# Kernel optimization log

Hardware: AMD Instinct MI355X
Metric: run time of the kernel (lower is better)

The kernel has to match this reference:

```python
import jax, jax.numpy as jnp
import numpy as np

N_HEADS = 8
HEAD_DIM = 32
KSIZE = 3
IN_CH = 128
OUT_CH = 256


def setup_inputs() -> dict:
    key = jax.random.key(0)
    k1, k2, k3, k4 = jax.random.split(key, 4)
    x = jax.random.normal(k1, (8, IN_CH, 64, 64), dtype=jnp.float32)
    w_key = jax.random.normal(k2, (N_HEADS * HEAD_DIM, IN_CH), dtype=jnp.float32) * 0.05
    b_key = jax.random.normal(k3, (N_HEADS * HEAD_DIM,), dtype=jnp.float32) * 0.05
    # memory init in torch: uniform in [-1, 1)
    memory = jax.random.uniform(k4, (N_HEADS, HEAD_DIM * KSIZE * KSIZE, OUT_CH // N_HEADS),
                                dtype=jnp.float32) * 2.0 - 1.0
    return {"x": x, "w_key": w_key, "b_key": b_key, "memory": memory}


def _unfold(z, k):
    # z: [b, C, Hp, Wp] padded; returns [b, C*k*k, H*W] with torch.unfold layout
    b, C, Hp, Wp = z.shape
    H, W = Hp - k + 1, Wp - k + 1
    patches = [z[:, :, i:i + H, j:j + W] for i in range(k) for j in range(k)]
    # stack -> [b, C, k*k, H, W]; channel-major like torch unfold (C outer, kh*k+kw inner)
    p = jnp.stack(patches, axis=2)
    return p.reshape(b, C * k * k, H * W)


def reference(x, w_key, b_key, memory):
    b, c_in, H, W = x.shape
    k = KSIZE
    m = N_HEADS
    # 1x1 conv (to_mem_key)
    key_map = jnp.einsum('oi,bihw->bohw', w_key, x) + b_key[None, :, None, None]
    # ZeroPad2d((k//2, k%2, k//2, k%2)) = (left, right, top, bottom)
    pl, pr = k // 2, k % 2
    padded = jnp.pad(key_map, ((0, 0), (0, 0), (pl, pr), (pl, pr)))
    unf = _unfold(padded, k)                      # [b, C*k*k, L], C = m*head_dim
    ckk = unf.shape[1]
    L = unf.shape[2]
    c = ckk // m
    # rearrange 'b (c m) l -> b m c l' (m is the FAST factor, per einops pattern)
    attn = unf.reshape(b, c, m, L).transpose(0, 2, 1, 3)   # [b, m, c, L]
    attn = jax.nn.softmax(attn, axis=2)
    out = jnp.einsum('nki,bnkl->bnil', memory, attn)       # [b, m, head_out, L]
    # rearrange 'b m c (h w) -> b (m c) h w'
    return out.reshape(b, m * out.shape[2], H, W)
```

## Files before the change

kernel.cpp:

```cpp
#include <hip/hip_runtime.h>
#include <hip/hip_bf16.h>

#define B_   8
#define CIN  128
#define CKEY 256
#define NH   8
#define HOUT 32
#define CPH  288
#define HW   4096

#define ESTR   264
#define EROW   (66 * ESTR)
#define E2_BYTES   (4 * EROW * 2)
#define XROW_DW    (64 * 68)
#define SMEM_BYTES E2_BYTES

typedef __attribute__((ext_vector_type(8))) short bf16x8;
typedef __attribute__((ext_vector_type(4))) float f32x4;

static __device__ __forceinline__ unsigned bfpack2(float a, float b) {
  __hip_bfloat162 h = __float22bfloat162_rn(float2{a, b});
  unsigned r;
  __builtin_memcpy(&r, &h, 4);
  return r;
}
static __device__ __forceinline__ unsigned short f2bf(float f) {
  unsigned u = __builtin_bit_cast(unsigned, f);
  u += 0x7FFFu + ((u >> 16) & 1u);
  return (unsigned short)(u >> 16);
}

__global__ __launch_bounds__(256) void prep_kernel(
    const float* __restrict__ mem, unsigned short* __restrict__ mfragP)
{
  const int idx  = blockIdx.x * 256 + threadIdx.x;
  const int lane = idx & 63, fi = idx >> 6;
  const int ib = fi & 1, pm = fi >> 1;
  const int p = pm % 9, m = pm / 9;
  const int li = lane & 15, q = lane >> 4;
  const int i = ib * 16 + li;
  unsigned short* dst = mfragP + (size_t)idx * 8;
#pragma unroll
  for (int j = 0; j < 8; ++j) {
    const int s = q * 8 + j;
    const int c = ((m - p + 8) & 7) + 8 * s;
    const int t = (9 * c + p) >> 3;
    dst[j] = f2bf(mem[((size_t)m * CPH + t) * HOUT + i]);
  }
}

__global__ __launch_bounds__(512) void fused_kernel(
    const float* __restrict__ x, const float* __restrict__ wk,
    const unsigned short* __restrict__ mfragP, const float* __restrict__ bk,
    float* __restrict__ out)
{
  extern __shared__ char smem[];
  unsigned short* e2 = (unsigned short*)smem;
  unsigned*       xdw = (unsigned*)smem;

  const int tid = threadIdx.x;
  const int bid = blockIdx.x;
  const int b  = bid & 7;
  const int h0 = (bid >> 3) * 2;
  const int lane = tid & 63;
  const int wv = __builtin_amdgcn_readfirstlane(tid >> 6);
  const int li = lane & 15, q = lane >> 4;

  float bias[2][4];
#pragma unroll
  for (int sh = 0; sh < 2; ++sh)
#pragma unroll
    for (int r = 0; r < 4; ++r)
      bias[sh][r] = bk[wv + 8 * (sh * 16 + 4 * q + r)];

  const int spx = tid & 63, sicg = tid >> 6;
  const int sxor = ((spx >> 3) & 7) << 3;

  const bool valid[4] = {h0 - 1 >= 0, true, true, h0 + 2 < 64};
  unsigned pk[4][8];
#pragma unroll
  for (int r = 0; r < 4; ++r) {
    if (!valid[r]) continue;
    const int y = h0 - 1 + r;
    const float* xr = x + (size_t)b * CIN * HW + y * 64 + spx;
#pragma unroll
    for (int r4 = 0; r4 < 4; ++r4) {
      const int ic0 = 4 * sicg + 32 * r4;
      const float v0 = xr[(size_t)(ic0 + 0) * HW];
      const float v1 = xr[(size_t)(ic0 + 1) * HW];
      const float v2 = xr[(size_t)(ic0 + 2) * HW];
      const float v3 = xr[(size_t)(ic0 + 3) * HW];
      pk[r][2 * r4 + 0] = bfpack2(v0, v1);
      pk[r][2 * r4 + 1] = bfpack2(v2, v3);
    }
  }

  bf16x8 wf[2][4];
#pragma unroll
  for (int sh = 0; sh < 2; ++sh)
#pragma unroll
    for (int ks = 0; ks < 4; ++ks) {
      const int och = wv + 8 * (sh * 16 + li);
      const float* src = wk + (size_t)och * CIN + ks * 32 + q * 8;
      const float4 v0 = *(const float4*)(src);
      const float4 v1 = *(const float4*)(src + 4);
      const int4 piv = make_int4(bfpack2(v0.x, v0.y), bfpack2(v0.z, v0.w),
                                 bfpack2(v1.x, v1.y), bfpack2(v1.z, v1.w));
      wf[sh][ks] = __builtin_bit_cast(bf16x8, piv);
    }

#pragma unroll
  for (int rr = 0; rr < 4; ++rr) {
    if (!valid[rr]) continue;
#pragma unroll
    for (int r4 = 0; r4 < 4; ++r4) {
      const int o = (2 * sicg + 16 * r4) ^ sxor;
      *(uint2*)(xdw + rr * XROW_DW + spx * 68 + o) =
          make_uint2(pk[rr][2 * r4], pk[rr][2 * r4 + 1]);
    }
  }
  __syncthreads();

  f32x4 acc[4][2][4];
#pragma unroll
  for (int rr = 0; rr < 4; ++rr)
#pragma unroll
    for (int sh = 0; sh < 2; ++sh)
#pragma unroll
      for (int pt = 0; pt < 4; ++pt) {
        f32x4 cv; cv[0] = bias[sh][0]; cv[1] = bias[sh][1];
        cv[2] = bias[sh][2]; cv[3] = bias[sh][3];
        acc[rr][sh][pt] = cv;
      }
#pragma unroll
  for (int ks = 0; ks < 4; ++ks) {
    const bf16x8 a0 = wf[0][ks];
    const bf16x8 a1 = wf[1][ks];
#pragma unroll
    for (int rr = 0; rr < 4; ++rr) {
      if (!valid[rr]) continue;
#pragma unroll
      for (int pt = 0; pt < 4; ++pt) {
        const int px  = pt * 16 + li;
        const int blk = (ks * 16 + q * 4) ^ (((px >> 3) & 7) << 3);
        const bf16x8 bfr = *(const bf16x8*)(xdw + rr * XROW_DW + px * 68 + blk);
        acc[rr][0][pt] = __builtin_amdgcn_mfma_f32_16x16x32_bf16(a0, bfr, acc[rr][0][pt], 0, 0, 0);
        acc[rr][1][pt] = __builtin_amdgcn_mfma_f32_16x16x32_bf16(a1, bfr, acc[rr][1][pt], 0, 0, 0);
      }
    }
  }
  __syncthreads();

#pragma unroll
  for (int rr = 0; rr < 4; ++rr) {
    if (!valid[rr]) continue;
    unsigned short* erow = e2 + rr * EROW;
#pragma unroll
    for (int sh = 0; sh < 2; ++sh)
#pragma unroll
      for (int pt = 0; pt < 4; ++pt) {
        const float w0 = __expf(acc[rr][sh][pt][0]);
        const float w1 = __expf(acc[rr][sh][pt][1]);
        const float w2 = __expf(acc[rr][sh][pt][2]);
        const float w3 = __expf(acc[rr][sh][pt][3]);
        unsigned short* dst = erow + (pt * 16 + li + 1) * ESTR
                            + wv * 32 + sh * 16 + 4 * q;
        *(uint2*)dst = make_uint2(bfpack2(w0, w1), bfpack2(w2, w3));
      }
    if (tid < 256) {
      const int xcol = (tid & 1) ? 65 : 0;
      ((unsigned*)(erow + xcol * ESTR))[tid >> 1] = 0x3F803F80u;
    }
  }
#pragma unroll
  for (int r = 0; r < 4; r += 3) {
    if (!valid[r]) {
      unsigned* erow = (unsigned*)(e2 + r * EROW);
      for (int d = tid; d < 66 * 132; d += 512) erow[d] = 0x3F803F80u;
    }
  }
  __syncthreads();

  const int m = wv;
  const unsigned short* mf = mfragP + (size_t)(m * 9) * 2 * 64 * 8;
  const int4 onesi = make_int4(0x3F803F80, 0x3F803F80, 0x3F803F80, 0x3F803F80);
  const bf16x8 bones = __builtin_bit_cast(bf16x8, onesi);

#pragma unroll
  for (int hh = 0; hh < 2; ++hh) {
    f32x4 acc2[4][2], accs[4];
#pragma unroll
    for (int pb = 0; pb < 4; ++pb) {
      acc2[pb][0] = {0.f, 0.f, 0.f, 0.f};
      acc2[pb][1] = {0.f, 0.f, 0.f, 0.f};
      accs[pb]    = {0.f, 0.f, 0.f, 0.f};
    }
#pragma unroll
    for (int p = 0; p < 9; ++p) {
      const bf16x8 bm0 = *(const bf16x8*)(mf + ((size_t)((p * 2 + 0) * 64 + lane)) * 8);
      const bf16x8 bm1 = *(const bf16x8*)(mf + ((size_t)((p * 2 + 1) * 64 + lane)) * 8);
      const int cmp  = (m - p + 8) & 7;
      const int rrow = hh + p / 3;
      const int dxp  = p - 3 * (p / 3);
      const unsigned short* abase = e2 + rrow * EROW + (li + dxp) * ESTR
                                  + cmp * 32 + q * 8;
#pragma unroll
      for (int pb = 0; pb < 4; ++pb) {
        const bf16x8 af = *(const bf16x8*)(abase + pb * 16 * ESTR);
        acc2[pb][0] = __builtin_amdgcn_mfma_f32_16x16x32_bf16(bm0, af, acc2[pb][0], 0, 0, 0);
        acc2[pb][1] = __builtin_amdgcn_mfma_f32_16x16x32_bf16(bm1, af, acc2[pb][1], 0, 0, 0);
        accs[pb]    = __builtin_amdgcn_mfma_f32_16x16x32_bf16(bones, af, accs[pb], 0, 0, 0);
      }
    }
    float* ob = out + ((size_t)(b * CKEY + m * HOUT)) * HW + (h0 + hh) * 64;
#pragma unroll
    for (int pb = 0; pb < 4; ++pb) {
      const float inv = 1.0f / accs[pb][0];
#pragma unroll
      for (int n = 0; n < 2; ++n)
#pragma unroll
        for (int r = 0; r < 4; ++r)
          ob[(size_t)(n * 16 + 4 * q + r) * HW + pb * 16 + li] =
              acc2[pb][n][r] * inv;
    }
  }
}

extern "C" void kernel_launch(void* const* d_in, const int* in_sizes, int n_in,
                              void* d_out, int out_size, void* d_ws, size_t ws_size,
                              hipStream_t stream) {
  const float* x   = (const float*)d_in[0];
  const float* wk  = (const float*)d_in[1];
  const float* bk  = (const float*)d_in[2];
  const float* mem = (const float*)d_in[3];

  unsigned short* mfragP = (unsigned short*)d_ws;

  (void)hipFuncSetAttribute((const void*)fused_kernel,
                            hipFuncAttributeMaxDynamicSharedMemorySize, SMEM_BYTES);

  prep_kernel<<<dim3(36), dim3(256), 0, stream>>>(mem, mfragP);
  fused_kernel<<<dim3(256), dim3(512), SMEM_BYTES, stream>>>(
      x, wk, mfragP, bk, (float*)d_out);
}
```

Measured before the change: 94.84 us.

## Split each row-pair tile into two column halves with halo to double grid

Each block now handles 32 output columns (plus a one-column halo) instead of all 64, so the grid grows from 256 to 512 blocks and the shared-memory footprint roughly halves. Launch bounds request 4 blocks per CU to raise occupancy. The cost is redundant key-conv work on halo columns (48 computed columns for 32 useful), a more complex strided x load with per-slot index math, and zero-fill of the padded columns in shared memory.

New measurement: 121.8 us. +28.5%, slower.

```diff
diff --git a/kernel.cpp b/kernel.cpp
--- a/kernel.cpp
+++ b/kernel.cpp
@@ -10,9 +10,11 @@
 #define HW   4096
 
 #define ESTR   264
-#define EROW   (66 * ESTR)
-#define E2_BYTES   (4 * EROW * 2)
-#define XROW_DW    (64 * 68)
+#define NCOL   34
+#define EROW2  (NCOL * ESTR)
+#define E2_BYTES (4 * EROW2 * 2)
+#define XCOL_DW 68
+#define XROW_DW (48 * XCOL_DW)
 #define SMEM_BYTES E2_BYTES
 
 typedef __attribute__((ext_vector_type(8))) short bf16x8;
@@ -49,7 +51,7 @@
   }
 }
 
-__global__ __launch_bounds__(512) void fused_kernel(
+__global__ __launch_bounds__(512, 4) void fused_kernel(
     const float* __restrict__ x, const float* __restrict__ wk,
     const unsigned short* __restrict__ mfragP, const float* __restrict__ bk,
     float* __restrict__ out)
@@ -61,7 +63,10 @@
   const int tid = threadIdx.x;
   const int bid = blockIdx.x;
   const int b  = bid & 7;
-  const int h0 = (bid >> 3) * 2;
+  const int t  = bid >> 3;
+  const int ph = t & 1;
+  const int h0 = (t >> 1) * 2;
+  const int P0 = ph * 32;
   const int lane = tid & 63;
   const int wv = __builtin_amdgcn_readfirstlane(tid >> 6);
   const int li = lane & 15, q = lane >> 4;
@@ -73,25 +78,31 @@
     for (int r = 0; r < 4; ++r)
       bias[sh][r] = bk[wv + 8 * (sh * 16 + 4 * q + r)];
 
-  const int spx = tid & 63, sicg = tid >> 6;
-  const int sxor = ((spx >> 3) & 7) << 3;
-
   const bool valid[4] = {h0 - 1 >= 0, true, true, h0 + 2 < 64};
-  unsigned pk[4][8];
-#pragma unroll
-  for (int r = 0; r < 4; ++r) {
-    if (!valid[r]) continue;
-    const int y = h0 - 1 + r;
-    const float* xr = x + (size_t)b * CIN * HW + y * 64 + spx;
-#pragma unroll
-    for (int r4 = 0; r4 < 4; ++r4) {
-      const int ic0 = 4 * sicg + 32 * r4;
-      const float v0 = xr[(size_t)(ic0 + 0) * HW];
-      const float v1 = xr[(size_t)(ic0 + 1) * HW];
-      const float v2 = xr[(size_t)(ic0 + 2) * HW];
-      const float v3 = xr[(size_t)(ic0 + 3) * HW];
-      pk[r][2 * r4 + 0] = bfpack2(v0, v1);
-      pk[r][2 * r4 + 1] = bfpack2(v2, v3);
+  const int cmin = ph ? 0 : 1;
+  const int cmax = ph ? 32 : 33;
+
+  unsigned pk[4][5];
+#pragma unroll
+  for (int rr = 0; rr < 4; ++rr) {
+    if (!valid[rr]) continue;
+    const int y = h0 - 1 + rr;
+    const float* xb = x + (size_t)b * CIN * HW + (size_t)y * 64;
+#pragma unroll
+    for (int it = 0; it < 5; ++it) {
+      const int slot = it * 512 + tid;
+      unsigned v = 0u;
+      if (slot < 64 * NCOL) {
+        const int icp = slot / NCOL;
+        const int c   = slot - icp * NCOL;
+        if (c >= cmin && c <= cmax) {
+          const int gpx = P0 - 1 + c;
+          const float v0 = xb[(size_t)(2 * icp) * HW + gpx];
+          const float v1 = xb[(size_t)(2 * icp + 1) * HW + gpx];
+          v = bfpack2(v0, v1);
+        }
+      }
+      pk[rr][it] = v;
     }
   }
 
@@ -109,25 +120,37 @@
       wf[sh][ks] = __builtin_bit_cast(bf16x8, piv);
     }
 
+  for (int d = tid; d < 4 * 14 * XCOL_DW; d += 512) {
+    const int rr  = d / (14 * XCOL_DW);
+    const int rem = d - rr * (14 * XCOL_DW);
+    const int ci  = rem / XCOL_DW;
+    const int o   = rem - ci * XCOL_DW;
+    xdw[rr * XROW_DW + (NCOL + ci) * XCOL_DW + o] = 0u;
+  }
+
 #pragma unroll
   for (int rr = 0; rr < 4; ++rr) {
     if (!valid[rr]) continue;
 #pragma unroll
-    for (int r4 = 0; r4 < 4; ++r4) {
-      const int o = (2 * sicg + 16 * r4) ^ sxor;
-      *(uint2*)(xdw + rr * XROW_DW + spx * 68 + o) =
-          make_uint2(pk[rr][2 * r4], pk[rr][2 * r4 + 1]);
+    for (int it = 0; it < 5; ++it) {
+      const int slot = it * 512 + tid;
+      if (slot < 64 * NCOL) {
+        const int icp = slot / NCOL;
+        const int c   = slot - icp * NCOL;
+        xdw[rr * XROW_DW + c * XCOL_DW + (icp ^ (((c >> 3) & 7) << 3))] =
+            pk[rr][it];
+      }
     }
   }
   __syncthreads();
 
-  f32x4 acc[4][2][4];
+  f32x4 acc[4][2][3];
 #pragma unroll
   for (int rr = 0; rr < 4; ++rr)
 #pragma unroll
     for (int sh = 0; sh < 2; ++sh)
 #pragma unroll
-      for (int pt = 0; pt < 4; ++pt) {
+      for (int pt = 0; pt < 3; ++pt) {
         f32x4 cv; cv[0] = bias[sh][0]; cv[1] = bias[sh][1];
         cv[2] = bias[sh][2]; cv[3] = bias[sh][3];
         acc[rr][sh][pt] = cv;
@@ -140,10 +163,10 @@
     for (int rr = 0; rr < 4; ++rr) {
       if (!valid[rr]) continue;
 #pragma unroll
-      for (int pt = 0; pt < 4; ++pt) {
-        const int px  = pt * 16 + li;
-        const int blk = (ks * 16 + q * 4) ^ (((px >> 3) & 7) << 3);
-        const bf16x8 bfr = *(const bf16x8*)(xdw + rr * XROW_DW + px * 68 + blk);
+      for (int pt = 0; pt < 3; ++pt) {
+        const int c   = pt * 16 + li;
+        const int blk = (ks * 16 + q * 4) ^ (((c >> 3) & 7) << 3);
+        const bf16x8 bfr = *(const bf16x8*)(xdw + rr * XROW_DW + c * XCOL_DW + blk);
         acc[rr][0][pt] = __builtin_amdgcn_mfma_f32_16x16x32_bf16(a0, bfr, acc[rr][0][pt], 0, 0, 0);
         acc[rr][1][pt] = __builtin_amdgcn_mfma_f32_16x16x32_bf16(a1, bfr, acc[rr][1][pt], 0, 0, 0);
       }
@@ -154,29 +177,31 @@
 #pragma unroll
   for (int rr = 0; rr < 4; ++rr) {
     if (!valid[rr]) continue;
-    unsigned short* erow = e2 + rr * EROW;
+    unsigned short* erow = e2 + rr * EROW2;
 #pragma unroll
     for (int sh = 0; sh < 2; ++sh)
 #pragma unroll
-      for (int pt = 0; pt < 4; ++pt) {
-        const float w0 = __expf(acc[rr][sh][pt][0]);
-        const float w1 = __expf(acc[rr][sh][pt][1]);
-        const float w2 = __expf(acc[rr][sh][pt][2]);
-        const float w3 = __expf(acc[rr][sh][pt][3]);
-        unsigned short* dst = erow + (pt * 16 + li + 1) * ESTR
-                            + wv * 32 + sh * 16 + 4 * q;
-        *(uint2*)dst = make_uint2(bfpack2(w0, w1), bfpack2(w2, w3));
-      }
-    if (tid < 256) {
-      const int xcol = (tid & 1) ? 65 : 0;
-      ((unsigned*)(erow + xcol * ESTR))[tid >> 1] = 0x3F803F80u;
+      for (int pt = 0; pt < 3; ++pt) {
+        const int ec = pt * 16 + li;
+        if (ec >= cmin && ec <= cmax) {
+          const float w0 = __expf(acc[rr][sh][pt][0]);
+          const float w1 = __expf(acc[rr][sh][pt][1]);
+          const float w2 = __expf(acc[rr][sh][pt][2]);
+          const float w3 = __expf(acc[rr][sh][pt][3]);
+          unsigned short* dst = erow + ec * ESTR + wv * 32 + sh * 16 + 4 * q;
+          *(uint2*)dst = make_uint2(bfpack2(w0, w1), bfpack2(w2, w3));
+        }
+      }
+    if (tid < 128) {
+      const int ec = ph ? 33 : 0;
+      ((unsigned*)(erow + ec * ESTR))[tid] = 0x3F803F80u;
     }
   }
 #pragma unroll
   for (int r = 0; r < 4; r += 3) {
     if (!valid[r]) {
-      unsigned* erow = (unsigned*)(e2 + r * EROW);
-      for (int d = tid; d < 66 * 132; d += 512) erow[d] = 0x3F803F80u;
+      unsigned* erow = (unsigned*)(e2 + r * EROW2);
+      for (int d = tid; d < NCOL * (ESTR / 2); d += 512) erow[d] = 0x3F803F80u;
     }
   }
   __syncthreads();
@@ -188,9 +213,9 @@
 
 #pragma unroll
   for (int hh = 0; hh < 2; ++hh) {
-    f32x4 acc2[4][2], accs[4];
-#pragma unroll
-    for (int pb = 0; pb < 4; ++pb) {
+    f32x4 acc2[2][2], accs[2];
+#pragma unroll
+    for (int pb = 0; pb < 2; ++pb) {
       acc2[pb][0] = {0.f, 0.f, 0.f, 0.f};
       acc2[pb][1] = {0.f, 0.f, 0.f, 0.f};
       accs[pb]    = {0.f, 0.f, 0.f, 0.f};
@@ -202,19 +227,19 @@
       const int cmp  = (m - p + 8) & 7;
       const int rrow = hh + p / 3;
       const int dxp  = p - 3 * (p / 3);
-      const unsigned short* abase = e2 + rrow * EROW + (li + dxp) * ESTR
+      const unsigned short* abase = e2 + rrow * EROW2 + (li + dxp) * ESTR
                                   + cmp * 32 + q * 8;
 #pragma unroll
-      for (int pb = 0; pb < 4; ++pb) {
+      for (int pb = 0; pb < 2; ++pb) {
         const bf16x8 af = *(const bf16x8*)(abase + pb * 16 * ESTR);
         acc2[pb][0] = __builtin_amdgcn_mfma_f32_16x16x32_bf16(bm0, af, acc2[pb][0], 0, 0, 0);
         acc2[pb][1] = __builtin_amdgcn_mfma_f32_16x16x32_bf16(bm1, af, acc2[pb][1], 0, 0, 0);
         accs[pb]    = __builtin_amdgcn_mfma_f32_16x16x32_bf16(bones, af, accs[pb], 0, 0, 0);
       }
     }
-    float* ob = out + ((size_t)(b * CKEY + m * HOUT)) * HW + (h0 + hh) * 64;
-#pragma unroll
-    for (int pb = 0; pb < 4; ++pb) {
+    float* ob = out + ((size_t)(b * CKEY + m * HOUT)) * HW + (h0 + hh) * 64 + P0;
+#pragma unroll
+    for (int pb = 0; pb < 2; ++pb) {
       const float inv = 1.0f / accs[pb][0];
 #pragma unroll
       for (int n = 0; n < 2; ++n)
@@ -240,6 +265,6 @@
                             hipFuncAttributeMaxDynamicSharedMemorySize, SMEM_BYTES);
 
   prep_kernel<<<dim3(36), dim3(256), 0, stream>>>(mem, mfragP);
-  fused_kernel<<<dim3(256), dim3(512), SMEM_BYTES, stream>>>(
+  fused_kernel<<<dim3(512), dim3(512), SMEM_BYTES, stream>>>(
       x, wk, mfragP, bk, (float*)d_out);
 }
```
